# Optimization experiments

Hardware: AMD Instinct MI355X
Metric: run time of the kernel (lower is better)

The kernel has to match this reference:

```python
import jax, jax.numpy as jnp
import numpy as np

N_INV, N_FUND = 100000, 20000
D_INV, D_FUND, H = 128, 64, 128
E, EL = 600000, 200000


def setup_inputs() -> dict:
    key = jax.random.key(0)
    ks = jax.random.split(key, 26)
    f = lambda k, shape: (jax.random.normal(k, shape, dtype=jnp.float32) * 0.05)
    inp = {
        'x_inv': jax.random.normal(ks[0], (N_INV, D_INV), dtype=jnp.float32),
        'x_fund': jax.random.normal(ks[1], (N_FUND, D_FUND), dtype=jnp.float32),
        'src_if': jax.random.randint(ks[2], (E,), 0, N_INV),
        'dst_if': jax.random.randint(ks[3], (E,), 0, N_FUND),
        'src_fi': jax.random.randint(ks[4], (E,), 0, N_FUND),
        'dst_fi': jax.random.randint(ks[5], (E,), 0, N_INV),
        'eli_inv': jax.random.randint(ks[6], (EL,), 0, N_INV),
        'eli_fund': jax.random.randint(ks[7], (EL,), 0, N_FUND),
        # layer-1 SAGEConv weights per relation (PyG: out = lin_l(mean(x_j)) + lin_r(x_dst))
        'W1l_if': f(ks[8], (H, D_INV)), 'b1_if': jnp.zeros((H,), jnp.float32), 'W1r_if': f(ks[9], (H, D_FUND)),
        'W1l_fi': f(ks[10], (H, D_FUND)), 'b1_fi': jnp.zeros((H,), jnp.float32), 'W1r_fi': f(ks[11], (H, D_INV)),
        # layer-2 SAGEConv weights per relation
        'W2l_if': f(ks[12], (H, H)), 'b2_if': jnp.zeros((H,), jnp.float32), 'W2r_if': f(ks[13], (H, H)),
        'W2l_fi': f(ks[14], (H, H)), 'b2_fi': jnp.zeros((H,), jnp.float32), 'W2r_fi': f(ks[15], (H, H)),
        # link predictor MLP
        'Wp1': f(ks[16], (H, 2 * H)), 'bp1': jnp.zeros((H,), jnp.float32),
        'Wp2': f(ks[17], (1, H)), 'bp2': jnp.zeros((1,), jnp.float32),
    }
    return inp


def _sage(x_src, x_dst, src, dst, n_dst, Wl, bl, Wr):
    # mean-aggregate neighbor messages, then lin_l(mean) + bias + lin_r(root)
    msg = x_src[src]                                              # [E, d_src]
    s = jax.ops.segment_sum(msg, dst, num_segments=n_dst)         # [n_dst, d_src]
    cnt = jax.ops.segment_sum(jnp.ones((src.shape[0],), x_src.dtype), dst, num_segments=n_dst)
    mean = s / jnp.maximum(cnt, 1.0)[:, None]                     # isolated nodes -> 0
    return mean @ Wl.T + bl + x_dst @ Wr.T


def reference(x_inv, x_fund, src_if, dst_if, src_fi, dst_fi, eli_inv, eli_fund,
              W1l_if, b1_if, W1r_if, W1l_fi, b1_fi, W1r_fi,
              W2l_if, b2_if, W2r_if, W2l_fi, b2_fi, W2r_fi,
              Wp1, bp1, Wp2, bp2):
    # layer 1 (hetero: one incoming relation per node type, aggr='sum' is identity)
    h_fund = jax.nn.relu(_sage(x_inv, x_fund, src_if, dst_if, N_FUND, W1l_if, b1_if, W1r_if))
    h_inv = jax.nn.relu(_sage(x_fund, x_inv, src_fi, dst_fi, N_INV, W1l_fi, b1_fi, W1r_fi))
    # layer 2
    z_fund = _sage(h_inv, h_fund, src_if, dst_if, N_FUND, W2l_if, b2_if, W2r_if)
    z_inv = _sage(h_fund, h_inv, src_fi, dst_fi, N_INV, W2l_fi, b2_fi, W2r_fi)
    # link predictor
    xi = z_inv[eli_inv]                                           # [EL, H]
    xj = z_fund[eli_fund]                                         # [EL, H]
    x = jnp.concatenate([xi, xj], axis=-1)                        # [EL, 2H]
    x = jax.nn.relu(x @ Wp1.T + bp1)
    return jax.nn.sigmoid(x @ Wp2.T + bp2)                        # [EL, 1]
```

## Files before the change

### kernel.cpp

```cpp
#include <hip/hip_runtime.h>
#include <cstdint>
#include <cstddef>

namespace {

typedef short bf16x8 __attribute__((ext_vector_type(8)));
typedef float f32x4 __attribute__((ext_vector_type(4)));

constexpr int kNInv  = 100000;
constexpr int kNFund = 20000;
constexpr int kH     = 128;
constexpr int kE     = 600000;
constexpr int kEL    = 200000;

constexpr int kW1lIF = 0;
constexpr int kW1rIF = 16384;
constexpr int kW1lFI = 24576;
constexpr int kW1rFI = 32768;
constexpr int kWTot  = 49152;

constexpr int kCW2lFI = 0;
constexpr int kCW2rFI = 16384;
constexpr int kCW2lIF = 32768;
constexpr int kCW2rIF = 49152;

__device__ __forceinline__ float bf_lo(uint32_t u) {
  union { uint32_t i; float f; } v; v.i = u << 16; return v.f;
}
__device__ __forceinline__ float bf_hi(uint32_t u) {
  union { uint32_t i; float f; } v; v.i = u & 0xffff0000u; return v.f;
}
__device__ __forceinline__ ushort f2bf(float f) {
  union { float f; uint32_t i; } v; v.f = f;
  uint32_t x = v.i;
  return (ushort)((x + 0x7fffu + ((x >> 16) & 1u)) >> 16);
}

constexpr int kXiQ = kNInv * 128 / 4;
constexpr int kXfQ = kNFund * 64 / 4;
constexpr int kWQ  = kWTot / 4;
constexpr int kTotQ = kXiQ + kXfQ + kWQ;
constexpr int kConvB = kTotQ / 256;
constexpr int kCountB = (2 * kE + 255) / 256;

__device__ __forceinline__ void count_body(int e,
                                           const int* __restrict__ dst_if,
                                           int* __restrict__ deg_fund, int* __restrict__ rank_if,
                                           const int* __restrict__ dst_fi,
                                           int* __restrict__ deg_inv, int* __restrict__ rank_fi) {
  if (e < kE) {
    rank_if[e] = atomicAdd(&deg_fund[dst_if[e]], 1);
  } else if (e < 2 * kE) {
    const int ee = e - kE;
    rank_fi[ee] = atomicAdd(&deg_inv[dst_fi[ee]], 1);
  }
}

__device__ void convert_body(int q, const float* __restrict__ xi, const float* __restrict__ xf,
                             const float* w0, const float* w1, const float* w2, const float* w3,
                             ushort* __restrict__ xi_b, ushort* __restrict__ xf_b,
                             ushort* __restrict__ wa) {
  const float* src;
  ushort* dst;
  int sidx, didx;
  if (q < kXiQ) {
    src = xi; dst = xi_b; sidx = q * 4; didx = q * 4;
  } else if (q < kXiQ + kXfQ) {
    src = xf; dst = xf_b; sidx = (q - kXiQ) * 4; didx = sidx;
  } else {
    const int e = (q - kXiQ - kXfQ) * 4;
    const float* ws[4] = {w0, w1, w2, w3};
    const int beg[5] = {kW1lIF, kW1rIF, kW1lFI, kW1rFI, kWTot};
    int s = 0;
    while (e >= beg[s + 1]) ++s;
    src = ws[s]; dst = wa; sidx = e - beg[s]; didx = e;
  }
  float4 v = *(const float4*)(src + sidx);
  ushort4 o = make_ushort4(f2bf(v.x), f2bf(v.y), f2bf(v.z), f2bf(v.w));
  *(ushort4*)(dst + didx) = o;
}

__device__ void composite_body(int b, const float* __restrict__ Wp1,
                               const float* __restrict__ W2l_fi, const float* __restrict__ W2r_fi,
                               const float* __restrict__ W2l_if, const float* __restrict__ W2r_if,
                               const float* __restrict__ b2_fi, const float* __restrict__ b2_if,
                               const float* __restrict__ bp1,
                               ushort* __restrict__ cw, float* __restrict__ bu_inv,
                               float* __restrict__ bu_fund, float* sA ) {
  const int tid = threadIdx.x;
  if (b == 16) {
    if (tid < 128) {
      float s = 0.f;
      for (int j = 0; j < 128; ++j) s += Wp1[(size_t)tid * 256 + j] * b2_fi[j];
      bu_inv[tid] = s;
    } else {
      const int o = tid - 128;
      float s = bp1[o];
      for (int j = 0; j < 128; ++j) s += Wp1[(size_t)o * 256 + 128 + j] * b2_if[j];
      bu_fund[o] = s;
    }
    return;
  }
  const int m = b >> 2;
  const int rb = (b & 3) * 32;
  const float* A = Wp1 + (m >= 2 ? 128 : 0);
  const float* B = (m == 0) ? W2l_fi : (m == 1) ? W2r_fi : (m == 2) ? W2l_if : W2r_if;
  for (int i = tid; i < 32 * 128; i += 256) {
    const int r = i >> 7, c = i & 127;
    sA[r * 132 + c] = A[(size_t)(rb + r) * 256 + c];
  }
  __syncthreads();
  const int lr = tid >> 3;
  const int k0 = (tid & 7) * 16;
  float acc[16];
#pragma unroll
  for (int i = 0; i < 16; ++i) acc[i] = 0.f;
  for (int j = 0; j < 128; ++j) {
    const float a = sA[lr * 132 + j];
    const float* Brow = B + (size_t)j * 128 + k0;
#pragma unroll
    for (int i = 0; i < 16; i += 4) {
      float4 v = *(const float4*)(Brow + i);
      acc[i] += a * v.x; acc[i + 1] += a * v.y; acc[i + 2] += a * v.z; acc[i + 3] += a * v.w;
    }
  }
  ushort* dst = cw + (size_t)m * 16384 + (size_t)(rb + lr) * 128 + k0;
  ushort ov[16];
#pragma unroll
  for (int i = 0; i < 16; ++i) ov[i] = f2bf(acc[i]);
#pragma unroll
  for (int i = 0; i < 16; i += 4)
    *(ushort4*)(dst + i) = *(const ushort4*)(ov + i);
}

__global__ __launch_bounds__(256) void prep(
    const int* dst_if, int* deg_fund, int* rank_if,
    const int* dst_fi, int* deg_inv, int* rank_fi,
    const float* xi, const float* xf,
    const float* w0, const float* w1, const float* w2, const float* w3,
    ushort* xi_b, ushort* xf_b, ushort* wa,
    const float* Wp1, const float* W2l_fi, const float* W2r_fi,
    const float* W2l_if, const float* W2r_if,
    const float* b2_fi, const float* b2_if, const float* bp1,
    ushort* cw, float* bu_inv, float* bu_fund) {
  __shared__ float smem[32 * 132];
  const int b = blockIdx.x;
  if (b < kCountB) {
    count_body(b * 256 + threadIdx.x, dst_if, deg_fund, rank_if, dst_fi, deg_inv, rank_fi);
  } else if (b < kCountB + kConvB) {
    convert_body((b - kCountB) * 256 + threadIdx.x, xi, xf, w0, w1, w2, w3, xi_b, xf_b, wa);
  } else {
    composite_body(b - kCountB - kConvB, Wp1, W2l_fi, W2r_fi, W2l_if, W2r_if,
                   b2_fi, b2_if, bp1, cw, bu_inv, bu_fund, smem);
  }
}


__device__ __forceinline__ void scan_partial_body(const int* __restrict__ deg,
                                                  int* __restrict__ bsum, int n, int blk) {
  __shared__ int red[256];
  const int tid = threadIdx.x;
  const int base = blk * 1024 + tid * 4;
  int s = 0;
  if (base + 3 < n) {
    int4 v = *(const int4*)(deg + base);
    s = v.x + v.y + v.z + v.w;
  } else {
    for (int i = 0; i < 4; ++i)
      if (base + i < n) s += deg[base + i];
  }
  red[tid] = s;
  __syncthreads();
  for (int d = 128; d > 0; d >>= 1) {
    if (tid < d) red[tid] += red[tid + d];
    __syncthreads();
  }
  if (tid == 0) bsum[blk] = red[0];
}

__global__ void scan_partial2(const int* __restrict__ degF, int* __restrict__ bsumF, int nF, int nbF,
                              const int* __restrict__ degI, int* __restrict__ bsumI, int nI) {
  if ((int)blockIdx.x < nbF) scan_partial_body(degF, bsumF, nF, blockIdx.x);
  else scan_partial_body(degI, bsumI, nI, blockIdx.x - nbF);
}

__device__ __forceinline__ void scan_apply_body(const int* __restrict__ deg,
                                                const int* __restrict__ bsum,
                                                int* __restrict__ off, int n, int blk) {
  __shared__ int red[256];
  __shared__ int sbase;
  const int tid = threadIdx.x;
  int part = 0;
  for (int i = tid; i < blk; i += 256) part += bsum[i];
  red[tid] = part;
  __syncthreads();
  for (int d = 128; d > 0; d >>= 1) {
    if (tid < d) red[tid] += red[tid + d];
    __syncthreads();
  }
  if (tid == 0) sbase = red[0];
  __syncthreads();
  const int base0 = sbase;
  __syncthreads();

  const int base = blk * 1024 + tid * 4;
  int v[4] = {0, 0, 0, 0};
  const bool full = (base + 3 < n);
  if (full) {
    int4 t = *(const int4*)(deg + base);
    v[0] = t.x; v[1] = t.y; v[2] = t.z; v[3] = t.w;
  } else {
    for (int i = 0; i < 4; ++i)
      if (base + i < n) v[i] = deg[base + i];
  }
  const int s = v[0] + v[1] + v[2] + v[3];
  red[tid] = s;
  __syncthreads();
  for (int d = 1; d < 256; d <<= 1) {
    int t = (tid >= d) ? red[tid - d] : 0;
    __syncthreads();
    red[tid] += t;
    __syncthreads();
  }
  int o[4];
  o[0] = base0 + red[tid] - s;
  o[1] = o[0] + v[0];
  o[2] = o[1] + v[1];
  o[3] = o[2] + v[2];
  if (full) {
    *(int4*)(off + base) = make_int4(o[0], o[1], o[2], o[3]);
  } else {
    for (int i = 0; i < 4; ++i)
      if (base + i < n) off[base + i] = o[i];
  }
#pragma unroll
  for (int i = 0; i < 4; ++i)
    if (base + i == n - 1) off[n] = o[i] + v[i];
}

__global__ void scan_apply2(const int* __restrict__ degF, const int* __restrict__ bsumF,
                            int* __restrict__ offF, int nF, int nbF,
                            const int* __restrict__ degI, const int* __restrict__ bsumI,
                            int* __restrict__ offI, int nI) {
  if ((int)blockIdx.x < nbF) scan_apply_body(degF, bsumF, offF, nF, blockIdx.x);
  else scan_apply_body(degI, bsumI, offI, nI, blockIdx.x - nbF);
}

__global__ void fill2(const int* __restrict__ s0, const int* __restrict__ d0,
                      const int* __restrict__ r0v, const int* __restrict__ off0,
                      int* __restrict__ c0,
                      const int* __restrict__ s1, const int* __restrict__ d1,
                      const int* __restrict__ r1v, const int* __restrict__ off1,
                      int* __restrict__ c1, int n) {
  int e = blockIdx.x * blockDim.x + threadIdx.x;
  if (e < n) {
    c0[off0[d0[e]] + r0v[e]] = s0[e];
  } else if (e < 2 * n) {
    int ee = e - n;
    c1[off1[d1[ee]] + r1v[ee]] = s1[ee];
  }
}


__device__ __forceinline__ void acc8w(float* a, uint4 u, float w) {
  a[0] = fmaf(w, bf_lo(u.x), a[0]); a[1] = fmaf(w, bf_hi(u.x), a[1]);
  a[2] = fmaf(w, bf_lo(u.y), a[2]); a[3] = fmaf(w, bf_hi(u.y), a[3]);
  a[4] = fmaf(w, bf_lo(u.z), a[4]); a[5] = fmaf(w, bf_hi(u.z), a[5]);
  a[6] = fmaf(w, bf_lo(u.w), a[6]); a[7] = fmaf(w, bf_hi(u.w), a[7]);
}

template <int D, int DEP>
__device__ __forceinline__ void mean_node(const ushort* __restrict__ xsrc,
                                          const int* __restrict__ csr,
                                          const int* __restrict__ off,
                                          ushort* __restrict__ mean, int node, int lane) {
  constexpr int NSUB = (D == 128) ? 4 : 8;
  const int sub = (D == 128) ? (lane >> 4) : (lane >> 3);
  const int ll  = (D == 128) ? (lane & 15) : (lane & 7);
  const size_t co = (size_t)ll * 8;
  const int lo = off[node], hi = off[node + 1];
  float a[8] = {0.f, 0.f, 0.f, 0.f, 0.f, 0.f, 0.f, 0.f};
  for (int e0 = lo + sub; e0 < hi; e0 += NSUB * DEP) {
    int idx[DEP];
    float w[DEP];
#pragma unroll
    for (int j = 0; j < DEP; ++j) {
      const int e = e0 + NSUB * j;
      idx[j] = csr[min(e, hi - 1)];
      w[j] = (e < hi) ? 1.0f : 0.0f;
    }
    uint4 u[DEP];
#pragma unroll
    for (int j = 0; j < DEP; ++j)
      u[j] = *(const uint4*)(xsrc + (size_t)idx[j] * D + co);
#pragma unroll
    for (int j = 0; j < DEP; ++j) acc8w(a, u[j], w[j]);
  }
#pragma unroll
  for (int i = 0; i < 8; ++i) {
    if (D == 64) a[i] += __shfl_xor(a[i], 8);
    a[i] += __shfl_xor(a[i], 16);
    a[i] += __shfl_xor(a[i], 32);
  }
  if (sub == 0) {
    const float sc = (hi > lo) ? 1.0f / (float)(hi - lo) : 0.0f;
    ushort o8[8];
#pragma unroll
    for (int i = 0; i < 8; ++i) o8[i] = f2bf(a[i] * sc);
    *(uint4*)(mean + (size_t)node * D + co) = *(const uint4*)o8;
  }
}

template <int DA, int DEPA, int DB, int DEPB>
__global__ void sage_mean_dual(const ushort* __restrict__ xA, const int* __restrict__ csrA,
                               const int* __restrict__ offA, ushort* __restrict__ outA, int nA,
                               const ushort* __restrict__ xB, const int* __restrict__ csrB,
                               const int* __restrict__ offB, ushort* __restrict__ outB, int nB) {
  const int wave = (int)((blockIdx.x * blockDim.x + threadIdx.x) >> 6);
  const int lane = threadIdx.x & 63;
  if (wave < nA) mean_node<DA, DEPA>(xA, csrA, offA, outA, wave, lane);
  else if (wave < nA + nB) mean_node<DB, DEPB>(xB, csrB, offB, outB, wave - nA, lane);
}


template <int D1, int D2>
__device__ void gemm_body(const ushort* __restrict__ A1, const ushort* __restrict__ A2,
                          const ushort* __restrict__ W1, const ushort* __restrict__ W2,
                          const float* __restrict__ bias, int act,
                          ushort* __restrict__ out, int n, int blk, ushort* lds) {
  constexpr int K1 = D1 / 32;
  constexpr int K2 = D2 / 32;
  constexpr int CH1 = 128 * D1 / 8;
  constexpr int CHT = 128 * (D1 + D2) / 8;

  const int tid = threadIdx.x;
  const int wid = tid >> 6;
  const int lane = tid & 63;
  const int lo16 = lane & 15;
  const int hi4 = lane >> 4;
  const int row0 = blk * 128 + wid * 32;

  const int r0 = min(row0 + lo16, n - 1);
  const int r1 = min(row0 + 16 + lo16, n - 1);

  bf16x8 aA[2][K1], aB[2][K2];
  {
    const ushort* a0p = A1 + (size_t)r0 * D1 + hi4 * 8;
    const ushort* a1p = A1 + (size_t)r1 * D1 + hi4 * 8;
#pragma unroll
    for (int k = 0; k < K1; ++k) {
      aA[0][k] = *(const bf16x8*)(a0p + k * 32);
      aA[1][k] = *(const bf16x8*)(a1p + k * 32);
    }
    const ushort* b0p = A2 + (size_t)r0 * D2 + hi4 * 8;
    const ushort* b1p = A2 + (size_t)r1 * D2 + hi4 * 8;
#pragma unroll
    for (int k = 0; k < K2; ++k) {
      aB[0][k] = *(const bf16x8*)(b0p + k * 32);
      aB[1][k] = *(const bf16x8*)(b1p + k * 32);
    }
  }

#pragma unroll
  for (int it = 0; it < CHT / 256; ++it) {
    const int c = it * 256 + tid;
    const int g = c * 8;
    bf16x8 v;
    int dest;
    if (g < 128 * D1) {
      const int row = g / D1, col = g % D1;
      v = *(const bf16x8*)(W1 + g);
      dest = ((col >> 5) * 8 + (row >> 4)) * 64 + (((col >> 3) & 3) << 4) + (row & 15);
    } else {
      const int g2 = g - 128 * D1;
      const int row = g2 / D2, col = g2 % D2;
      v = *(const bf16x8*)(W2 + g2);
      dest = CH1 + ((col >> 5) * 8 + (row >> 4)) * 64 + (((col >> 3) & 3) << 4) + (row & 15);
    }
    *((bf16x8*)lds + dest) = v;
  }
  __syncthreads();

  f32x4 acc[2][8];
#pragma unroll
  for (int rt = 0; rt < 2; ++rt)
#pragma unroll
    for (int ct = 0; ct < 8; ++ct)
      acc[rt][ct] = (f32x4){0.f, 0.f, 0.f, 0.f};

  const bf16x8* fr = (const bf16x8*)lds;
#pragma unroll
  for (int k = 0; k < K1; ++k) {
#pragma unroll
    for (int ct = 0; ct < 8; ++ct) {
      bf16x8 w = fr[(k * 8 + ct) * 64 + lane];
      acc[0][ct] = __builtin_amdgcn_mfma_f32_16x16x32_bf16(w, aA[0][k], acc[0][ct], 0, 0, 0);
      acc[1][ct] = __builtin_amdgcn_mfma_f32_16x16x32_bf16(w, aA[1][k], acc[1][ct], 0, 0, 0);
    }
  }
#pragma unroll
  for (int k = 0; k < K2; ++k) {
#pragma unroll
    for (int ct = 0; ct < 8; ++ct) {
      bf16x8 w = fr[CH1 + (k * 8 + ct) * 64 + lane];
      acc[0][ct] = __builtin_amdgcn_mfma_f32_16x16x32_bf16(w, aB[0][k], acc[0][ct], 0, 0, 0);
      acc[1][ct] = __builtin_amdgcn_mfma_f32_16x16x32_bf16(w, aB[1][k], acc[1][ct], 0, 0, 0);
    }
  }

  const int colb = hi4 * 4;
#pragma unroll
  for (int rt = 0; rt < 2; ++rt) {
    const int row = row0 + rt * 16 + lo16;
    if (row < n) {
#pragma unroll
      for (int ct = 0; ct < 8; ++ct) {
        float b4[4];
        *(float4*)b4 = *(const float4*)(bias + ct * 16 + colb);
        ushort o[4];
#pragma unroll
        for (int j = 0; j < 4; ++j) {
          float x = acc[rt][ct][j] + b4[j];
          if (act) x = fmaxf(x, 0.f);
          o[j] = f2bf(x);
        }
        *(ushort4*)(out + (size_t)row * kH + ct * 16 + colb) = *(const ushort4*)o;
      }
    }
  }
}

__global__ __launch_bounds__(256) void gemm_stage1(
    const ushort* A1f, const ushort* A2f, const ushort* W1f, const ushort* W2f,
    const float* biasf, ushort* outf, int nf, int nbf,
    const ushort* A1i, const ushort* A2i, const ushort* W1i, const ushort* W2i,
    const float* biasi, ushort* outi, int ni) {
  __shared__ ushort lds[128 * 192];
  if ((int)blockIdx.x < nbf)
    gemm_body<128, 64>(A1f, A2f, W1f, W2f, biasf, 1, outf, nf, blockIdx.x, lds);
  else
    gemm_body<64, 128>(A1i, A2i, W1i, W2i, biasi, 1, outi, ni, blockIdx.x - nbf, lds);
}

__global__ __launch_bounds__(256) void gemm_stage2(
    const ushort* A1f, const ushort* A2f, const ushort* W1f, const ushort* W2f,
    const float* biasf, ushort* outf, int nf, int nbf,
    const ushort* A1i, const ushort* A2i, const ushort* W1i, const ushort* W2i,
    const float* biasi, ushort* outi, int ni) {
  __shared__ ushort lds[128 * 256];
  if ((int)blockIdx.x < nbf)
    gemm_body<128, 128>(A1f, A2f, W1f, W2f, biasf, 0, outf, nf, blockIdx.x, lds);
  else
    gemm_body<128, 128>(A1i, A2i, W1i, W2i, biasi, 0, outi, ni, blockIdx.x - nbf, lds);
}


__global__ void link_pred(const ushort* __restrict__ u_inv, const ushort* __restrict__ u_fund,
                          const int* __restrict__ ei, const int* __restrict__ ej,
                          const float* __restrict__ Wp2, const float* __restrict__ bp2,
                          float* __restrict__ out, int nl) {
  const int wave = (int)((blockIdx.x * blockDim.x + threadIdx.x) >> 6);
  const int lane = threadIdx.x & 63;
  const int q = lane >> 4, l16 = lane & 15;
  const int link = wave * 4 + q;
  if (link >= nl) return;
  const int i = ei[link];
  const int j = ej[link];
  uint4 ua = *(const uint4*)(u_inv + (size_t)i * 128 + l16 * 8);
  uint4 ub = *(const uint4*)(u_fund + (size_t)j * 128 + l16 * 8);
  float4 w0 = *(const float4*)(Wp2 + l16 * 8);
  float4 w1 = *(const float4*)(Wp2 + l16 * 8 + 4);
  float p = fmaxf(bf_lo(ua.x) + bf_lo(ub.x), 0.f) * w0.x
          + fmaxf(bf_hi(ua.x) + bf_hi(ub.x), 0.f) * w0.y
          + fmaxf(bf_lo(ua.y) + bf_lo(ub.y), 0.f) * w0.z
          + fmaxf(bf_hi(ua.y) + bf_hi(ub.y), 0.f) * w0.w
          + fmaxf(bf_lo(ua.z) + bf_lo(ub.z), 0.f) * w1.x
          + fmaxf(bf_hi(ua.z) + bf_hi(ub.z), 0.f) * w1.y
          + fmaxf(bf_lo(ua.w) + bf_lo(ub.w), 0.f) * w1.z
          + fmaxf(bf_hi(ua.w) + bf_hi(ub.w), 0.f) * w1.w;
#pragma unroll
  for (int o = 8; o > 0; o >>= 1) p += __shfl_xor(p, o);
  if (l16 == 0) out[link] = 1.0f / (1.0f + expf(-(p + bp2[0])));
}

}

extern "C" void kernel_launch(void* const* d_in, const int* in_sizes, int n_in,
                              void* d_out, int out_size, void* d_ws, size_t ws_size,
                              hipStream_t stream) {
  const float* x_inv  = (const float*)d_in[0];
  const float* x_fund = (const float*)d_in[1];
  const int* src_if   = (const int*)d_in[2];
  const int* dst_if   = (const int*)d_in[3];
  const int* src_fi   = (const int*)d_in[4];
  const int* dst_fi   = (const int*)d_in[5];
  const int* eli_inv  = (const int*)d_in[6];
  const int* eli_fund = (const int*)d_in[7];
  const float* W1l_if = (const float*)d_in[8];
  const float* b1_if  = (const float*)d_in[9];
  const float* W1r_if = (const float*)d_in[10];
  const float* W1l_fi = (const float*)d_in[11];
  const float* b1_fi  = (const float*)d_in[12];
  const float* W1r_fi = (const float*)d_in[13];
  const float* W2l_if = (const float*)d_in[14];
  const float* b2_if  = (const float*)d_in[15];
  const float* W2r_if = (const float*)d_in[16];
  const float* W2l_fi = (const float*)d_in[17];
  const float* b2_fi  = (const float*)d_in[18];
  const float* W2r_fi = (const float*)d_in[19];
  const float* Wp1    = (const float*)d_in[20];
  const float* bp1    = (const float*)d_in[21];
  const float* Wp2    = (const float*)d_in[22];
  const float* bp2    = (const float*)d_in[23];
  float* out = (float*)d_out;

  char* p = (char*)d_ws;
  auto alloc = [&](size_t bytes) -> void* {
    void* r = (void*)p;
    p += (bytes + 255) & ~(size_t)255;
    return r;
  };
  int* deg_fund = (int*)alloc((size_t)kNFund * 4);
  int* deg_inv  = (int*)alloc((size_t)kNInv * 4);
  int* off_fund = (int*)alloc((size_t)(kNFund + 1) * 4);
  int* off_inv  = (int*)alloc((size_t)(kNInv + 1) * 4);
  int* bsumF    = (int*)alloc((size_t)1024 * 4);
  int* bsumI    = (int*)alloc((size_t)1024 * 4);
  int* rank_if  = (int*)alloc((size_t)kE * 4);
  int* rank_fi  = (int*)alloc((size_t)kE * 4);
  int* csr_if   = (int*)alloc((size_t)kE * 4);
  int* csr_fi   = (int*)alloc((size_t)kE * 4);
  ushort* xi_b = (ushort*)alloc((size_t)kNInv * 128 * 2);
  ushort* xf_b = (ushort*)alloc((size_t)kNFund * 64 * 2);
  ushort* wa   = (ushort*)alloc((size_t)kWTot * 2);
  ushort* cw   = (ushort*)alloc((size_t)4 * 16384 * 2);
  float* bu_inv  = (float*)alloc((size_t)128 * 4);
  float* bu_fund = (float*)alloc((size_t)128 * 4);
  ushort* bufA = (ushort*)alloc((size_t)kNFund * 128 * 2);
  ushort* bufB = (ushort*)alloc((size_t)kNFund * 128 * 2);
  ushort* bufC = (ushort*)alloc((size_t)kNInv * 128 * 2);
  ushort* bufD = (ushort*)alloc((size_t)kNInv * 128 * 2);
  ushort* bufE = (ushort*)alloc((size_t)kNFund * 128 * 2);
  ushort* bufF = (ushort*)alloc((size_t)kNInv * 128 * 2);

  const int TB = 256;
  const int nbFund = (kNFund + 1023) / 1024;
  const int nbInv  = (kNInv + 1023) / 1024;
  const int gemmF = (kNFund + 127) / 128;
  const int gemmI = (kNInv + 127) / 128;

  hipMemsetAsync(deg_fund, 0, (size_t)kNFund * 4, stream);
  hipMemsetAsync(deg_inv, 0, (size_t)kNInv * 4, stream);

  prep<<<kCountB + kConvB + 17, 256, 0, stream>>>(
      dst_if, deg_fund, rank_if, dst_fi, deg_inv, rank_fi,
      x_inv, x_fund, W1l_if, W1r_if, W1l_fi, W1r_fi, xi_b, xf_b, wa,
      Wp1, W2l_fi, W2r_fi, W2l_if, W2r_if, b2_fi, b2_if, bp1, cw, bu_inv, bu_fund);

  scan_partial2<<<nbFund + nbInv, 256, 0, stream>>>(deg_fund, bsumF, kNFund, nbFund,
                                                    deg_inv, bsumI, kNInv);
  scan_apply2<<<nbFund + nbInv, 256, 0, stream>>>(deg_fund, bsumF, off_fund, kNFund, nbFund,
                                                  deg_inv, bsumI, off_inv, kNInv);

  fill2<<<(2 * kE + TB - 1) / TB, TB, 0, stream>>>(
      src_if, dst_if, rank_if, off_fund, csr_if,
      src_fi, dst_fi, rank_fi, off_inv, csr_fi, kE);

  const int meanBlocks = (kNFund + kNInv + 3) / 4;

  sage_mean_dual<128, 4, 64, 2><<<meanBlocks, 256, 0, stream>>>(
      xi_b, csr_if, off_fund, bufA, kNFund, xf_b, csr_fi, off_inv, bufC, kNInv);
  gemm_stage1<<<gemmF + gemmI, 256, 0, stream>>>(
      bufA, xf_b, wa + kW1lIF, wa + kW1rIF, b1_if, bufB, kNFund, gemmF,
      bufC, xi_b, wa + kW1lFI, wa + kW1rFI, b1_fi, bufD, kNInv);
  sage_mean_dual<128, 4, 128, 2><<<meanBlocks, 256, 0, stream>>>(
      bufD, csr_if, off_fund, bufA, kNFund, bufB, csr_fi, off_inv, bufC, kNInv);
  gemm_stage2<<<gemmF + gemmI, 256, 0, stream>>>(
      bufA, bufB, cw + kCW2lIF, cw + kCW2rIF, bu_fund, bufE, kNFund, gemmF,
      bufC, bufD, cw + kCW2lFI, cw + kCW2rFI, bu_inv, bufF, kNInv);
  link_pred<<<(kEL / 4 + 3) / 4, 256, 0, stream>>>(bufF, bufE, eli_inv, eli_fund,
                                                   Wp2, bp2, out, kEL);
}
```

Baseline: 303.2 us.

## Fuse neighbor mean aggregation into SAGE GEMM kernels via LDS tiles

Replaces the separate mean-aggregation kernels and GEMM kernels with fused per-layer kernels. Each block gathers and averages neighbor rows for its 128 nodes into LDS, then runs MFMA with weights read directly from global memory instead of staged in LDS. The degree counting is split back out of the prep kernel into its own launch. This removes the intermediate mean buffers and their round trip through memory, but changes gather parallelism: each node now uses one thread group walking edges serially, and weight fragments are re-fetched from global/L2 per block.

```diff
diff --git a/kernel.cpp b/kernel.cpp
--- a/kernel.cpp
+++ b/kernel.cpp
@@ -41,20 +41,6 @@
 constexpr int kWQ  = kWTot / 4;
 constexpr int kTotQ = kXiQ + kXfQ + kWQ;
 constexpr int kConvB = kTotQ / 256;
-constexpr int kCountB = (2 * kE + 255) / 256;
-
-__device__ __forceinline__ void count_body(int e,
-                                           const int* __restrict__ dst_if,
-                                           int* __restrict__ deg_fund, int* __restrict__ rank_if,
-                                           const int* __restrict__ dst_fi,
-                                           int* __restrict__ deg_inv, int* __restrict__ rank_fi) {
-  if (e < kE) {
-    rank_if[e] = atomicAdd(&deg_fund[dst_if[e]], 1);
-  } else if (e < 2 * kE) {
-    const int ee = e - kE;
-    rank_fi[ee] = atomicAdd(&deg_inv[dst_fi[ee]], 1);
-  }
-}
 
 __device__ void convert_body(int q, const float* __restrict__ xi, const float* __restrict__ xf,
                              const float* w0, const float* w1, const float* w2, const float* w3,
@@ -134,8 +120,6 @@
 }
 
 __global__ __launch_bounds__(256) void prep(
-    const int* dst_if, int* deg_fund, int* rank_if,
-    const int* dst_fi, int* deg_inv, int* rank_fi,
     const float* xi, const float* xf,
     const float* w0, const float* w1, const float* w2, const float* w3,
     ushort* xi_b, ushort* xf_b, ushort* wa,
@@ -145,13 +129,24 @@
     ushort* cw, float* bu_inv, float* bu_fund) {
   __shared__ float smem[32 * 132];
   const int b = blockIdx.x;
-  if (b < kCountB) {
-    count_body(b * 256 + threadIdx.x, dst_if, deg_fund, rank_if, dst_fi, deg_inv, rank_fi);
-  } else if (b < kCountB + kConvB) {
-    convert_body((b - kCountB) * 256 + threadIdx.x, xi, xf, w0, w1, w2, w3, xi_b, xf_b, wa);
+  if (b < kConvB) {
+    convert_body(b * 256 + threadIdx.x, xi, xf, w0, w1, w2, w3, xi_b, xf_b, wa);
   } else {
-    composite_body(b - kCountB - kConvB, Wp1, W2l_fi, W2r_fi, W2l_if, W2r_if,
+    composite_body(b - kConvB, Wp1, W2l_fi, W2r_fi, W2l_if, W2r_if,
                    b2_fi, b2_if, bp1, cw, bu_inv, bu_fund, smem);
+  }
+}
+
+__global__ void count_rank2(const int* __restrict__ d0, int* __restrict__ g0,
+                            int* __restrict__ r0v,
+                            const int* __restrict__ d1, int* __restrict__ g1,
+                            int* __restrict__ r1v, int n) {
+  int e = blockIdx.x * blockDim.x + threadIdx.x;
+  if (e < n) {
+    r0v[e] = atomicAdd(&g0[d0[e]], 1);
+  } else if (e < 2 * n) {
+    int ee = e - n;
+    r1v[ee] = atomicAdd(&g1[d1[ee]], 1);
   }
 }
 
@@ -269,91 +264,80 @@
   a[6] = fmaf(w, bf_lo(u.w), a[6]); a[7] = fmaf(w, bf_hi(u.w), a[7]);
 }
 
-template <int D, int DEP>
-__device__ __forceinline__ void mean_node(const ushort* __restrict__ xsrc,
-                                          const int* __restrict__ csr,
-                                          const int* __restrict__ off,
-                                          ushort* __restrict__ mean, int node, int lane) {
-  constexpr int NSUB = (D == 128) ? 4 : 8;
-  const int sub = (D == 128) ? (lane >> 4) : (lane >> 3);
-  const int ll  = (D == 128) ? (lane & 15) : (lane & 7);
-  const size_t co = (size_t)ll * 8;
-  const int lo = off[node], hi = off[node + 1];
-  float a[8] = {0.f, 0.f, 0.f, 0.f, 0.f, 0.f, 0.f, 0.f};
-  for (int e0 = lo + sub; e0 < hi; e0 += NSUB * DEP) {
-    int idx[DEP];
-    float w[DEP];
-#pragma unroll
-    for (int j = 0; j < DEP; ++j) {
-      const int e = e0 + NSUB * j;
-      idx[j] = csr[min(e, hi - 1)];
-      w[j] = (e < hi) ? 1.0f : 0.0f;
-    }
-    uint4 u[DEP];
-#pragma unroll
-    for (int j = 0; j < DEP; ++j)
-      u[j] = *(const uint4*)(xsrc + (size_t)idx[j] * D + co);
-#pragma unroll
-    for (int j = 0; j < DEP; ++j) acc8w(a, u[j], w[j]);
-  }
-#pragma unroll
-  for (int i = 0; i < 8; ++i) {
-    if (D == 64) a[i] += __shfl_xor(a[i], 8);
-    a[i] += __shfl_xor(a[i], 16);
-    a[i] += __shfl_xor(a[i], 32);
-  }
-  if (sub == 0) {
-    const float sc = (hi > lo) ? 1.0f / (float)(hi - lo) : 0.0f;
-    ushort o8[8];
-#pragma unroll
-    for (int i = 0; i < 8; ++i) o8[i] = f2bf(a[i] * sc);
-    *(uint4*)(mean + (size_t)node * D + co) = *(const uint4*)o8;
-  }
-}
-
-template <int DA, int DEPA, int DB, int DEPB>
-__global__ void sage_mean_dual(const ushort* __restrict__ xA, const int* __restrict__ csrA,
-                               const int* __restrict__ offA, ushort* __restrict__ outA, int nA,
-                               const ushort* __restrict__ xB, const int* __restrict__ csrB,
-                               const int* __restrict__ offB, ushort* __restrict__ outB, int nB) {
-  const int wave = (int)((blockIdx.x * blockDim.x + threadIdx.x) >> 6);
-  const int lane = threadIdx.x & 63;
-  if (wave < nA) mean_node<DA, DEPA>(xA, csrA, offA, outA, wave, lane);
-  else if (wave < nA + nB) mean_node<DB, DEPB>(xB, csrB, offB, outB, wave - nA, lane);
-}
-
-
-template <int D1, int D2>
-__device__ void gemm_body(const ushort* __restrict__ A1, const ushort* __restrict__ A2,
-                          const ushort* __restrict__ W1, const ushort* __restrict__ W2,
-                          const float* __restrict__ bias, int act,
-                          ushort* __restrict__ out, int n, int blk, ushort* lds) {
+template <int D1, int DEPA, int D2>
+__device__ void fused_layer_body(
+    const ushort* __restrict__ gtab, const int* __restrict__ csr, const int* __restrict__ off,
+    const ushort* __restrict__ root,
+    const ushort* __restrict__ W1, const ushort* __restrict__ W2,
+    const float* __restrict__ bias, int act,
+    ushort* __restrict__ out, int n, int blk, ushort* lds_a) {
+  constexpr int LDA = D1 + 8;
   constexpr int K1 = D1 / 32;
   constexpr int K2 = D2 / 32;
-  constexpr int CH1 = 128 * D1 / 8;
-  constexpr int CHT = 128 * (D1 + D2) / 8;
-
   const int tid = threadIdx.x;
+  const int row0 = blk * 128;
+
+  {
+    constexpr int GL = (D1 == 128) ? 16 : 8;
+    constexpr int NG = 256 / GL;
+    const int grp = tid / GL;
+    const int ll = tid % GL;
+    const size_t co = (size_t)ll * 8;
+    for (int r = grp; r < 128; r += NG) {
+      const int node = min(row0 + r, n - 1);
+      const int lo = off[node], hi = off[node + 1];
+      float a[8] = {0.f, 0.f, 0.f, 0.f, 0.f, 0.f, 0.f, 0.f};
+      for (int e0 = lo; e0 < hi; e0 += DEPA) {
+        int idx[DEPA];
+        float w[DEPA];
+#pragma unroll
+        for (int j = 0; j < DEPA; ++j) {
+          const int e = e0 + j;
+          idx[j] = csr[min(e, hi - 1)];
+          w[j] = (e < hi) ? 1.0f : 0.0f;
+        }
+        uint4 u[DEPA];
+#pragma unroll
+        for (int j = 0; j < DEPA; ++j)
+          u[j] = *(const uint4*)(gtab + (size_t)idx[j] * D1 + co);
+#pragma unroll
+        for (int j = 0; j < DEPA; ++j) acc8w(a, u[j], w[j]);
+      }
+      const float sc = (hi > lo) ? 1.0f / (float)(hi - lo) : 0.0f;
+      ushort o8[8];
+#pragma unroll
+      for (int i = 0; i < 8; ++i) o8[i] = f2bf(a[i] * sc);
+      *(uint4*)&lds_a[(size_t)r * LDA + co] = *(const uint4*)o8;
+    }
+  }
+  __syncthreads();
+
   const int wid = tid >> 6;
   const int lane = tid & 63;
   const int lo16 = lane & 15;
   const int hi4 = lane >> 4;
-  const int row0 = blk * 128 + wid * 32;
-
-  const int r0 = min(row0 + lo16, n - 1);
-  const int r1 = min(row0 + 16 + lo16, n - 1);
-
-  bf16x8 aA[2][K1], aB[2][K2];
+  const int rl0 = wid * 32 + lo16;
+  const int rl1 = rl0 + 16;
+  const int r0g = min(row0 + rl0, n - 1);
+  const int r1g = min(row0 + rl1, n - 1);
+
+  f32x4 acc[2][8];
+#pragma unroll
+  for (int rt = 0; rt < 2; ++rt)
+#pragma unroll
+    for (int ct = 0; ct < 8; ++ct)
+      acc[rt][ct] = (f32x4){0.f, 0.f, 0.f, 0.f};
+
+  bf16x8 aA[2][K1];
+#pragma unroll
+  for (int k = 0; k < K1; ++k) {
+    aA[0][k] = *(const bf16x8*)&lds_a[(size_t)rl0 * LDA + k * 32 + hi4 * 8];
+    aA[1][k] = *(const bf16x8*)&lds_a[(size_t)rl1 * LDA + k * 32 + hi4 * 8];
+  }
+  bf16x8 aB[2][K2];
   {
-    const ushort* a0p = A1 + (size_t)r0 * D1 + hi4 * 8;
-    const ushort* a1p = A1 + (size_t)r1 * D1 + hi4 * 8;
-#pragma unroll
-    for (int k = 0; k < K1; ++k) {
-      aA[0][k] = *(const bf16x8*)(a0p + k * 32);
-      aA[1][k] = *(const bf16x8*)(a1p + k * 32);
-    }
-    const ushort* b0p = A2 + (size_t)r0 * D2 + hi4 * 8;
-    const ushort* b1p = A2 + (size_t)r1 * D2 + hi4 * 8;
+    const ushort* b0p = root + (size_t)r0g * D2 + hi4 * 8;
+    const ushort* b1p = root + (size_t)r1g * D2 + hi4 * 8;
 #pragma unroll
     for (int k = 0; k < K2; ++k) {
       aB[0][k] = *(const bf16x8*)(b0p + k * 32);
@@ -361,48 +345,22 @@
     }
   }
 
-#pragma unroll
-  for (int it = 0; it < CHT / 256; ++it) {
-    const int c = it * 256 + tid;
-    const int g = c * 8;
-    bf16x8 v;
-    int dest;
-    if (g < 128 * D1) {
-      const int row = g / D1, col = g % D1;
-      v = *(const bf16x8*)(W1 + g);
-      dest = ((col >> 5) * 8 + (row >> 4)) * 64 + (((col >> 3) & 3) << 4) + (row & 15);
-    } else {
-      const int g2 = g - 128 * D1;
-      const int row = g2 / D2, col = g2 % D2;
-      v = *(const bf16x8*)(W2 + g2);
-      dest = CH1 + ((col >> 5) * 8 + (row >> 4)) * 64 + (((col >> 3) & 3) << 4) + (row & 15);
-    }
-    *((bf16x8*)lds + dest) = v;
-  }
-  __syncthreads();
-
-  f32x4 acc[2][8];
-#pragma unroll
-  for (int rt = 0; rt < 2; ++rt)
-#pragma unroll
-    for (int ct = 0; ct < 8; ++ct)
-      acc[rt][ct] = (f32x4){0.f, 0.f, 0.f, 0.f};
-
-  const bf16x8* fr = (const bf16x8*)lds;
+  const ushort* wp1 = W1 + (size_t)lo16 * D1 + hi4 * 8;
 #pragma unroll
   for (int k = 0; k < K1; ++k) {
 #pragma unroll
     for (int ct = 0; ct < 8; ++ct) {
-      bf16x8 w = fr[(k * 8 + ct) * 64 + lane];
+      bf16x8 w = *(const bf16x8*)(wp1 + (size_t)ct * 16 * D1 + k * 32);
       acc[0][ct] = __builtin_amdgcn_mfma_f32_16x16x32_bf16(w, aA[0][k], acc[0][ct], 0, 0, 0);
       acc[1][ct] = __builtin_amdgcn_mfma_f32_16x16x32_bf16(w, aA[1][k], acc[1][ct], 0, 0, 0);
     }
   }
+  const ushort* wp2 = W2 + (size_t)lo16 * D2 + hi4 * 8;
 #pragma unroll
   for (int k = 0; k < K2; ++k) {
 #pragma unroll
     for (int ct = 0; ct < 8; ++ct) {
-      bf16x8 w = fr[CH1 + (k * 8 + ct) * 64 + lane];
+      bf16x8 w = *(const bf16x8*)(wp2 + (size_t)ct * 16 * D2 + k * 32);
       acc[0][ct] = __builtin_amdgcn_mfma_f32_16x16x32_bf16(w, aB[0][k], acc[0][ct], 0, 0, 0);
       acc[1][ct] = __builtin_amdgcn_mfma_f32_16x16x32_bf16(w, aB[1][k], acc[1][ct], 0, 0, 0);
     }
@@ -411,7 +369,7 @@
   const int colb = hi4 * 4;
 #pragma unroll
   for (int rt = 0; rt < 2; ++rt) {
-    const int row = row0 + rt * 16 + lo16;
+    const int row = row0 + (rt ? rl1 : rl0);
     if (row < n) {
 #pragma unroll
       for (int ct = 0; ct < 8; ++ct) {
@@ -430,28 +388,32 @@
   }
 }
 
-__global__ __launch_bounds__(256) void gemm_stage1(
-    const ushort* A1f, const ushort* A2f, const ushort* W1f, const ushort* W2f,
-    const float* biasf, ushort* outf, int nf, int nbf,
-    const ushort* A1i, const ushort* A2i, const ushort* W1i, const ushort* W2i,
-    const float* biasi, ushort* outi, int ni) {
-  __shared__ ushort lds[128 * 192];
+__global__ __launch_bounds__(256) void fused_layer1(
+    const ushort* xi_b, const int* csr_if, const int* off_fund, const ushort* xf_b,
+    const ushort* W1lif, const ushort* W1rif, const float* b1if, ushort* outF, int nbf,
+    const int* csr_fi, const int* off_inv,
+    const ushort* W1lfi, const ushort* W1rfi, const float* b1fi, ushort* outI) {
+  __shared__ ushort lds_a[128 * 136];
   if ((int)blockIdx.x < nbf)
-    gemm_body<128, 64>(A1f, A2f, W1f, W2f, biasf, 1, outf, nf, blockIdx.x, lds);
+    fused_layer_body<128, 8, 64>(xi_b, csr_if, off_fund, xf_b, W1lif, W1rif, b1if, 1,
+                                 outF, kNFund, blockIdx.x, lds_a);
   else
-    gemm_body<64, 128>(A1i, A2i, W1i, W2i, biasi, 1, outi, ni, blockIdx.x - nbf, lds);
-}
-
-__global__ __launch_bounds__(256) void gemm_stage2(
-    const ushort* A1f, const ushort* A2f, const ushort* W1f, const ushort* W2f,
-    const float* biasf, ushort* outf, int nf, int nbf,
-    const ushort* A1i, const ushort* A2i, const ushort* W1i, const ushort* W2i,
-    const float* biasi, ushort* outi, int ni) {
-  __shared__ ushort lds[128 * 256];
+    fused_layer_body<64, 4, 128>(xf_b, csr_fi, off_inv, xi_b, W1lfi, W1rfi, b1fi, 1,
+                                 outI, kNInv, blockIdx.x - nbf, lds_a);
+}
+
+__global__ __launch_bounds__(256) void fused_layer2(
+    const ushort* hinv, const int* csr_if, const int* off_fund, const ushort* hfund,
+    const ushort* cWlif, const ushort* cWrif, const float* buF, ushort* outF, int nbf,
+    const int* csr_fi, const int* off_inv,
+    const ushort* cWlfi, const ushort* cWrfi, const float* buI, ushort* outI) {
+  __shared__ ushort lds_a[128 * 136];
   if ((int)blockIdx.x < nbf)
-    gemm_body<128, 128>(A1f, A2f, W1f, W2f, biasf, 0, outf, nf, blockIdx.x, lds);
+    fused_layer_body<128, 8, 128>(hinv, csr_if, off_fund, hfund, cWlif, cWrif, buF, 0,
+                                  outF, kNFund, blockIdx.x, lds_a);
   else
-    gemm_body<128, 128>(A1i, A2i, W1i, W2i, biasi, 0, outi, ni, blockIdx.x - nbf, lds);
+    fused_layer_body<128, 4, 128>(hfund, csr_fi, off_inv, hinv, cWlfi, cWrfi, buI, 0,
+                                  outI, kNInv, blockIdx.x - nbf, lds_a);
 }
 
 
@@ -536,9 +498,7 @@
   ushort* cw   = (ushort*)alloc((size_t)4 * 16384 * 2);
   float* bu_inv  = (float*)alloc((size_t)128 * 4);
   float* bu_fund = (float*)alloc((size_t)128 * 4);
-  ushort* bufA = (ushort*)alloc((size_t)kNFund * 128 * 2);
   ushort* bufB = (ushort*)alloc((size_t)kNFund * 128 * 2);
-  ushort* bufC = (ushort*)alloc((size_t)kNInv * 128 * 2);
   ushort* bufD = (ushort*)alloc((size_t)kNInv * 128 * 2);
   ushort* bufE = (ushort*)alloc((size_t)kNFund * 128 * 2);
   ushort* bufF = (ushort*)alloc((size_t)kNInv * 128 * 2);
@@ -552,10 +512,12 @@
   hipMemsetAsync(deg_fund, 0, (size_t)kNFund * 4, stream);
   hipMemsetAsync(deg_inv, 0, (size_t)kNInv * 4, stream);
 
-  prep<<<kCountB + kConvB + 17, 256, 0, stream>>>(
-      dst_if, deg_fund, rank_if, dst_fi, deg_inv, rank_fi,
+  prep<<<kConvB + 17, 256, 0, stream>>>(
       x_inv, x_fund, W1l_if, W1r_if, W1l_fi, W1r_fi, xi_b, xf_b, wa,
       Wp1, W2l_fi, W2r_fi, W2l_if, W2r_if, b2_fi, b2_if, bp1, cw, bu_inv, bu_fund);
+
+  count_rank2<<<(2 * kE + TB - 1) / TB, TB, 0, stream>>>(
+      dst_if, deg_fund, rank_if, dst_fi, deg_inv, rank_fi, kE);
 
   scan_partial2<<<nbFund + nbInv, 256, 0, stream>>>(deg_fund, bsumF, kNFund, nbFund,
                                                     deg_inv, bsumI, kNInv);
@@ -566,18 +528,14 @@
       src_if, dst_if, rank_if, off_fund, csr_if,
       src_fi, dst_fi, rank_fi, off_inv, csr_fi, kE);
 
-  const int meanBlocks = (kNFund + kNInv + 3) / 4;
-
-  sage_mean_dual<128, 4, 64, 2><<<meanBlocks, 256, 0, stream>>>(
-      xi_b, csr_if, off_fund, bufA, kNFund, xf_b, csr_fi, off_inv, bufC, kNInv);
-  gemm_stage1<<<gemmF + gemmI, 256, 0, stream>>>(
-      bufA, xf_b, wa + kW1lIF, wa + kW1rIF, b1_if, bufB, kNFund, gemmF,
-      bufC, xi_b, wa + kW1lFI, wa + kW1rFI, b1_fi, bufD, kNInv);
-  sage_mean_dual<128, 4, 128, 2><<<meanBlocks, 256, 0, stream>>>(
-      bufD, csr_if, off_fund, bufA, kNFund, bufB, csr_fi, off_inv, bufC, kNInv);
-  gemm_stage2<<<gemmF + gemmI, 256, 0, stream>>>(
-      bufA, bufB, cw + kCW2lIF, cw + kCW2rIF, bu_fund, bufE, kNFund, gemmF,
-      bufC, bufD, cw + kCW2lFI, cw + kCW2rFI, bu_inv, bufF, kNInv);
+  fused_layer1<<<gemmF + gemmI, 256, 0, stream>>>(
+      xi_b, csr_if, off_fund, xf_b, wa + kW1lIF, wa + kW1rIF, b1_if, bufB, gemmF,
+      csr_fi, off_inv, wa + kW1lFI, wa + kW1rFI, b1_fi, bufD);
+
+  fused_layer2<<<gemmF + gemmI, 256, 0, stream>>>(
+      bufD, csr_if, off_fund, bufB, cw + kCW2lIF, cw + kCW2rIF, bu_fund, bufE, gemmF,
+      csr_fi, off_inv, cw + kCW2lFI, cw + kCW2rFI, bu_inv, bufF);
+
   link_pred<<<(kEL / 4 + 3) / 4, 256, 0, stream>>>(bufF, bufE, eli_inv, eli_fund,
                                                    Wp2, bp2, out, kEL);
 }
```

New measurement: 321.7 us. 1.06x slower.
